# Performance work log

Hardware: AMD Instinct MI355X
Metric: run time of the kernel (lower is better)

The kernel has to match this reference:

```python
import jax, jax.numpy as jnp
import numpy as np

B, L, C, H = 8, 1024, 1024, 16  # batch, seq_len, n_embed, n_head


def setup_inputs() -> dict:
    key = jax.random.key(0)
    k0, k1, k2 = jax.random.split(key, 3)
    s = 0.02  # init scale
    return {
        "x": jax.random.normal(k0, (B, L, C), jnp.float32),
        "W_qkv": jax.random.normal(k1, (C, 3 * C), jnp.float32) * s,  # (in, out) layout
        "b_qkv": jnp.zeros((3 * C,), jnp.float32),
        "W_proj": jax.random.normal(k2, (C, C), jnp.float32) * s,
        "b_proj": jnp.zeros((C,), jnp.float32),
    }


def reference(x, W_qkv, b_qkv, W_proj, b_proj):
    Bb, Ll, Cc = x.shape
    d = Cc // H  # head dim
    qkv = x @ W_qkv + b_qkv                      # (B, L, 3C)
    q, k, v = jnp.split(qkv, 3, axis=2)
    q = q.reshape(Bb, Ll, H, d).transpose(0, 2, 1, 3)  # (B, H, L, d)
    k = k.reshape(Bb, Ll, H, d).transpose(0, 2, 1, 3)
    v = v.reshape(Bb, Ll, H, d).transpose(0, 2, 1, 3)
    scale = 1.0 / np.sqrt(d).astype(np.float32)
    attn = jnp.einsum("bhid,bhjd->bhij", q, k) * scale  # (B, H, Lq, Lk)
    causal = jnp.tril(jnp.ones((Ll, Ll), dtype=bool))    # (Lq, Lk)
    attn = jnp.where(causal[None, None, :, :], attn, -jnp.inf)
    # NOTE: source uses F.softmax(attn, dim=2) -> softmax over the QUERY axis.
    attn = jax.nn.softmax(attn, axis=2)
    y = jnp.einsum("bhij,bhjd->bhid", attn, v)           # (B, H, L, d)
    y = y.transpose(0, 2, 1, 3).reshape(Bb, Ll, Cc)      # (B, L, C)
    return y @ W_proj + b_proj
```

## Files before the change

### kernel.cpp

```cpp
#include <hip/hip_runtime.h>

typedef unsigned short u16;
typedef unsigned int   u32;
using bf16x8 = __attribute__((ext_vector_type(8))) short;
using f32x4  = __attribute__((ext_vector_type(4))) float;
using f32x16 = __attribute__((ext_vector_type(16))) float;
using u32x4  = __attribute__((ext_vector_type(4))) u32;

static constexpr int Bb = 8, Ll = 1024, Cc = 1024, Hh = 16, Dd = 64;
static constexpr int Mrows = Bb * Ll;
static constexpr int N3    = 3 * Cc;
static constexpr float QSCALE = 0.125f * 1.44269504088896f;

__device__ __forceinline__ u16 f2b(float f) {
    u32 u = __builtin_bit_cast(u32, f);
    u += 0x7FFFu + ((u >> 16) & 1u);
    return (u16)(u >> 16);
}
__device__ __forceinline__ float b2f(u16 u) {
    return __builtin_bit_cast(float, (u32)u << 16);
}
__device__ __forceinline__ u32 pack2bf(float a, float b) {
    return (u32)f2b(a) | ((u32)f2b(b) << 16);
}
__device__ __forceinline__ void gload16(const u16* g, u16* l) {
    __builtin_amdgcn_global_load_lds(
        (const __attribute__((address_space(1))) void*)g,
        (__attribute__((address_space(3))) void*)l, 16, 0, 0);
}

__global__ void k_f32_to_bf16(const float* __restrict__ in, u16* __restrict__ out, int n16) {
    int idx = blockIdx.x * blockDim.x + threadIdx.x;
    if (idx >= n16) return;
    #pragma unroll
    for (int h = 0; h < 2; ++h) {
        f32x4 v0 = *((const f32x4*)in + idx * 4 + h * 2);
        f32x4 v1 = *((const f32x4*)in + idx * 4 + h * 2 + 1);
        u32x4 o;
        o[0] = pack2bf(v0[0], v0[1]);
        o[1] = pack2bf(v0[2], v0[3]);
        o[2] = pack2bf(v1[0], v1[1]);
        o[3] = pack2bf(v1[2], v1[3]);
        *((u32x4*)out + idx * 2 + h) = o;
    }
}

__global__ void k_transpose_w(const float* __restrict__ Wqkv, u16* __restrict__ WqkvT,
                              const float* __restrict__ Wproj, u16* __restrict__ WprojT) {
    __shared__ float tile[32][33];
    int bx = blockIdx.x;
    const float* in; u16* out; int Cn;
    if (bx < 96) { in = Wqkv;  out = WqkvT;  Cn = N3; }
    else         { in = Wproj; out = WprojT; Cn = Cc; bx -= 96; }
    const int R = Cc;
    int tx = threadIdx.x, ty = threadIdx.y;
    int c = bx * 32 + tx;
    int rbase = blockIdx.y * 32;
    #pragma unroll
    for (int rr = 0; rr < 4; ++rr)
        tile[ty + rr * 8][tx] = in[(size_t)(rbase + ty + rr * 8) * Cn + c];
    __syncthreads();
    int ro = bx * 32 + ty;
    #pragma unroll
    for (int rr = 0; rr < 4; ++rr)
        out[(size_t)(ro + rr * 8) * R + rbase + tx] = f2b(tile[tx][ty + rr * 8]);
}

__global__ void k_transpose_scale_bf16(const u16* __restrict__ in, const float* __restrict__ zinv,
                                       u16* __restrict__ out, int R, int Cn) {
    __shared__ u16 tile[32][33];
    int bh = blockIdx.z;
    size_t base = (size_t)bh * R * Cn;
    int tx = threadIdx.x, ty = threadIdx.y;
    int c = blockIdx.x * 32 + tx;
    int rbase = blockIdx.y * 32;
    #pragma unroll
    for (int rr = 0; rr < 4; ++rr)
        tile[ty + rr * 8][tx] = in[base + (size_t)(rbase + ty + rr * 8) * Cn + c];
    __syncthreads();
    float zv = zinv[(size_t)bh * R + rbase + tx];
    int ro = blockIdx.x * 32 + ty;
    #pragma unroll
    for (int rr = 0; rr < 4; ++rr)
        out[base + (size_t)(ro + rr * 8) * R + rbase + tx] = f2b(b2f(tile[tx][ty + rr * 8]) * zv);
}

__global__ __launch_bounds__(256, 2)
void k_gemm_qkv32(const u16* __restrict__ A, const u16* __restrict__ Bt,
                  const float* __restrict__ bias,
                  u16* __restrict__ qo, u16* __restrict__ ko, u16* __restrict__ vo)
{
    const int K = Cc;
    const int NT = K / 64;
    __shared__ u16 As[2][128 * 64];
    __shared__ u16 Bs[2][128 * 64];
    const int tid = threadIdx.x;
    const int wid = tid >> 6, lane = tid & 63;
    const int l31 = lane & 31, lhi = lane >> 5, l7 = lane & 7;
    const int wr = wid >> 1, wc = wid & 1;
    const int nwg = gridDim.x * gridDim.y;
    const int flat = blockIdx.y * gridDim.x + blockIdx.x;
    const int swz = (flat & 7) * (nwg >> 3) + (flat >> 3);
    const int bx = swz % gridDim.x, by = swz / gridDim.x;
    const int row0 = by * 128, col0 = bx * 128;

    const int srow = tid >> 3;
    const int schunk = (tid & 7) ^ (srow & 7);
    const u16* gA = A  + (size_t)(row0 + srow) * K + schunk * 8;
    const u16* gB = Bt + (size_t)(col0 + srow) * K + schunk * 8;

#define STG(buf, t) do { \
    const u16* ga_ = gA + (size_t)(t) * 64; \
    const u16* gb_ = gB + (size_t)(t) * 64; \
    u16* la_ = &As[buf][wid * 512]; \
    u16* lb_ = &Bs[buf][wid * 512]; \
    gload16(ga_,                  la_); \
    gload16(ga_ + (size_t)32 * K, la_ + 2048); \
    gload16(ga_ + (size_t)64 * K, la_ + 4096); \
    gload16(ga_ + (size_t)96 * K, la_ + 6144); \
    gload16(gb_,                  lb_); \
    gload16(gb_ + (size_t)32 * K, lb_ + 2048); \
    gload16(gb_ + (size_t)64 * K, lb_ + 4096); \
    gload16(gb_ + (size_t)96 * K, lb_ + 6144); \
} while (0)

    const int coff0 = (((0 + lhi) ^ l7) << 3);
    const int coff1 = (((2 + lhi) ^ l7) << 3);
    const int coff2 = (((4 + lhi) ^ l7) << 3);
    const int coff3 = (((6 + lhi) ^ l7) << 3);
    const int coff[4] = { coff0, coff1, coff2, coff3 };

    f32x16 acc[2][2] = {};

    STG(0, 0);
    STG(1, 1);
    asm volatile("s_waitcnt vmcnt(8)" ::: "memory");
    __builtin_amdgcn_s_barrier();
    __builtin_amdgcn_sched_barrier(0);

    for (int t = 0; t < NT; ++t) {
        const u16* cA = &As[t & 1][0];
        const u16* cB = &Bs[t & 1][0];
        bf16x8 af[2][4], bf0[4];
        #pragma unroll
        for (int tm = 0; tm < 2; ++tm)
            #pragma unroll
            for (int kc = 0; kc < 4; ++kc)
                af[tm][kc] = *(const bf16x8*)&cA[(wr * 64 + tm * 32 + l31) * 64 + coff[kc]];
        #pragma unroll
        for (int kc = 0; kc < 4; ++kc)
            bf0[kc] = *(const bf16x8*)&cB[(wc * 64 + l31) * 64 + coff[kc]];
        __builtin_amdgcn_s_setprio(1);
        #pragma unroll
        for (int tm = 0; tm < 2; ++tm)
            #pragma unroll
            for (int kc = 0; kc < 4; ++kc)
                acc[tm][0] = __builtin_amdgcn_mfma_f32_32x32x16_bf16(
                    af[tm][kc], bf0[kc], acc[tm][0], 0, 0, 0);
        __builtin_amdgcn_s_setprio(0);
        __builtin_amdgcn_s_barrier();
        bf16x8 bf1[4];
        #pragma unroll
        for (int kc = 0; kc < 4; ++kc)
            bf1[kc] = *(const bf16x8*)&cB[(wc * 64 + 32 + l31) * 64 + coff[kc]];
        __builtin_amdgcn_s_setprio(1);
        #pragma unroll
        for (int tm = 0; tm < 2; ++tm)
            #pragma unroll
            for (int kc = 0; kc < 4; ++kc)
                acc[tm][1] = __builtin_amdgcn_mfma_f32_32x32x16_bf16(
                    af[tm][kc], bf1[kc], acc[tm][1], 0, 0, 0);
        __builtin_amdgcn_s_setprio(0);
        __builtin_amdgcn_s_barrier();
        __builtin_amdgcn_sched_barrier(0);
        if (t + 2 < NT) STG(t & 1, t + 2);
        if (t + 1 < NT) {
            if (t + 2 < NT) { asm volatile("s_waitcnt vmcnt(8)" ::: "memory"); }
            else            { asm volatile("s_waitcnt vmcnt(0)" ::: "memory"); }
            __builtin_amdgcn_s_barrier();
            __builtin_amdgcn_sched_barrier(0);
        }
    }
#undef STG

    #pragma unroll
    for (int tm = 0; tm < 2; ++tm) {
        #pragma unroll
        for (int tn = 0; tn < 2; ++tn) {
            int cg = col0 + wc * 64 + tn * 32 + l31;
            float bv = bias[cg];
            int which = cg >> 10;
            float sc = (which == 0) ? QSCALE : 1.0f;
            int cc2 = cg & 1023;
            int h = cc2 >> 6, dd = cc2 & 63;
            int rbase = row0 + wr * 64 + tm * 32 + 4 * lhi;
            #pragma unroll
            for (int g = 0; g < 4; ++g) {
                #pragma unroll
                for (int r = 0; r < 4; ++r) {
                    int rg = rbase + 8 * g + r;
                    int bidx = rg >> 10, ll2 = rg & 1023;
                    size_t o = ((size_t)(bidx * Hh + h) * Ll + ll2) * Dd + dd;
                    u16 val = f2b((acc[tm][tn][g * 4 + r] + bv) * sc);
                    if (which == 0) qo[o] = val;
                    else if (which == 1) ko[o] = val;
                    else vo[o] = val;
                }
            }
        }
    }
}

__global__ __launch_bounds__(256)
void k_gemm_proj(const u16* __restrict__ A, const u16* __restrict__ Bt,
                 const float* __restrict__ bias, float* __restrict__ outf)
{
    const int N = Cc, K = Cc;
    __shared__ u16 As[2][128 * 32];
    __shared__ u16 Bs[2][128 * 32];
    const int tid = threadIdx.x;
    const int wid = tid >> 6, lane = tid & 63;
    const int lr = lane & 15, lg = lane >> 4;
    const int wr = wid >> 1, wc = wid & 1;
    const int nwg = gridDim.x * gridDim.y;
    const int flat = blockIdx.y * gridDim.x + blockIdx.x;
    const int swz = (flat & 7) * (nwg >> 3) + (flat >> 3);
    const int bx = swz % gridDim.x, by = swz / gridDim.x;
    const int row0 = by * 128, col0 = bx * 128;

    const int srow = wid * 32 + (lane >> 2);
    const int schk = (lane & 3) ^ (srow & 3);
    const u16* aP = A  + (size_t)(row0 + srow) * K + schk * 8;
    const u16* bP = Bt + (size_t)(col0 + srow) * K + schk * 8;
    const size_t r16 = (size_t)16 * K;
    u16* aL0 = &As[0][wid * 32 * 32]; u16* aL0b = aL0 + 16 * 32;
    u16* bL0 = &Bs[0][wid * 32 * 32]; u16* bL0b = bL0 + 16 * 32;
    u16* aL1 = &As[1][wid * 32 * 32]; u16* aL1b = aL1 + 16 * 32;
    u16* bL1 = &Bs[1][wid * 32 * 32]; u16* bL1b = bL1 + 16 * 32;

    f32x4 acc[4][4] = {};

#define STAGE0(kk) { gload16(aP + (kk), aL0); gload16(aP + r16 + (kk), aL0b); \
                     gload16(bP + (kk), bL0); gload16(bP + r16 + (kk), bL0b); }
#define STAGE1(kk) { gload16(aP + (kk), aL1); gload16(aP + r16 + (kk), aL1b); \
                     gload16(bP + (kk), bL1); gload16(bP + r16 + (kk), bL1b); }
#define COMPUTE(bufi) { \
        bf16x8 af[4], bfv[4]; \
        _Pragma("unroll") \
        for (int m = 0; m < 4; ++m) { int rw = wr * 64 + m * 16 + lr; \
            af[m] = *(const bf16x8*)&As[bufi][rw * 32 + ((lg ^ (rw & 3)) * 8)]; } \
        _Pragma("unroll") \
        for (int n = 0; n < 4; ++n) { int rw = wc * 64 + n * 16 + lr; \
            bfv[n] = *(const bf16x8*)&Bs[bufi][rw * 32 + ((lg ^ (rw & 3)) * 8)]; } \
        _Pragma("unroll") \
        for (int m = 0; m < 4; ++m) \
            _Pragma("unroll") \
            for (int n = 0; n < 4; ++n) \
                acc[m][n] = __builtin_amdgcn_mfma_f32_16x16x32_bf16(af[m], bfv[n], acc[m][n], 0, 0, 0); }

    STAGE0(0);
    __syncthreads();
    for (int k0 = 0; k0 < K; k0 += 64) {
        if (k0 + 32 < K) STAGE1(k0 + 32);
        COMPUTE(0);
        __syncthreads();
        if (k0 + 64 < K) STAGE0(k0 + 64);
        COMPUTE(1);
        __syncthreads();
    }
#undef STAGE0
#undef STAGE1
#undef COMPUTE

    #pragma unroll
    for (int m = 0; m < 4; ++m) {
        int rb2 = row0 + wr * 64 + m * 16 + lg * 4;
        #pragma unroll
        for (int n = 0; n < 4; ++n) {
            int cg = col0 + wc * 64 + n * 16 + lr;
            float bv = bias[cg];
            #pragma unroll
            for (int r = 0; r < 4; ++r)
                outf[(size_t)(rb2 + r) * N + cg] = acc[m][n][r] + bv;
        }
    }
}

__global__ __launch_bounds__(256, 4)
void k_attn_colsum(const u16* __restrict__ Q, const u16* __restrict__ Kb,
                   float* __restrict__ zinv)
{
    __shared__ u16 Qs[2][64 * 64];
    const int tid = threadIdx.x;
    const int wid = tid >> 6, lane = tid & 63;
    const int lr = lane & 15, lg = lane >> 4;
    const int l7 = lr & 7;
    const int fid = blockIdx.x;
    const int xcd = fid & 7, n = fid >> 3;
    const int xtA = n & 7;
    const int xtB = 15 - xtA;
    const int bh = (xcd << 4) | (n >> 3);
    const u16* Qp = Q  + (size_t)bh * Ll * Dd;
    const u16* Kp = Kb + (size_t)bh * Ll * Dd;
    const int jwA = xtA * 64 + wid * 16;
    const int jwB = xtB * 64 + wid * 16;
    bf16x8 kbA0 = *(const bf16x8*)&Kp[(jwA + lr) * Dd + lg * 8];
    bf16x8 kbA1 = *(const bf16x8*)&Kp[(jwA + lr) * Dd + 32 + lg * 8];
    bf16x8 kbB0 = *(const bf16x8*)&Kp[(jwB + lr) * Dd + lg * 8];
    bf16x8 kbB1 = *(const bf16x8*)&Kp[(jwB + lr) * Dd + 32 + lg * 8];
    const bool dmask[4] = { lg * 4 + 0 >= lr, lg * 4 + 1 >= lr,
                            lg * 4 + 2 >= lr, lg * 4 + 3 >= lr };
    const int ch0 = ((lg ^ l7) << 3);
    const int ch1 = (((4 + lg) ^ l7) << 3);
    const int srow = tid >> 3;
    const int schunk = (tid & 7) ^ (srow & 7);
    float zA = 0.f, zB = 0.f;

    const int nA = 16 - xtA;
    const int NS = 17;
#define IOF(s) (((s) < nA) ? (xtA * 64 + 64 * (s)) : (xtB * 64 + 64 * ((s) - nA)))

#define STGQ(buf, I0) do { \
    const u16* g_ = Qp + (size_t)((I0) + srow) * 64 + schunk * 8; \
    u16* l_ = &Qs[buf][wid * 512]; \
    gload16(g_,                   l_); \
    gload16(g_ + (size_t)32 * 64, l_ + 2048); \
} while (0)

#define CS_STEP(buf, I0, JW, KB0, KB1, ZACC) do { \
    const u16* Qs_ = &Qs[buf][0]; \
    _Pragma("unroll") \
    for (int ss = 0; ss < 4; ++ss) { \
        int ib = (I0) + ss * 16; \
        if (ib >= (JW)) { \
            bf16x8 qa0 = *(const bf16x8*)&Qs_[(ss * 16 + lr) * 64 + ch0]; \
            bf16x8 qa1 = *(const bf16x8*)&Qs_[(ss * 16 + lr) * 64 + ch1]; \
            f32x4 s_ = {0.f, 0.f, 0.f, 0.f}; \
            s_ = __builtin_amdgcn_mfma_f32_16x16x32_bf16(qa0, KB0, s_, 0, 0, 0); \
            s_ = __builtin_amdgcn_mfma_f32_16x16x32_bf16(qa1, KB1, s_, 0, 0, 0); \
            if (ib >= (JW) + 16) { \
                _Pragma("unroll") \
                for (int r = 0; r < 4; ++r) ZACC += exp2f(s_[r]); \
            } else { \
                _Pragma("unroll") \
                for (int r = 0; r < 4; ++r) ZACC += dmask[r] ? exp2f(s_[r]) : 0.f; \
            } \
        } \
    } \
} while (0)

    STGQ(0, IOF(0));
    STGQ(1, IOF(1));
    asm volatile("s_waitcnt vmcnt(2)" ::: "memory");
    __builtin_amdgcn_s_barrier();
    __builtin_amdgcn_sched_barrier(0);

    for (int s = 0; s < NS; ++s) {
        if (s < nA) { CS_STEP((s & 1), xtA * 64 + 64 * s, jwA, kbA0, kbA1, zA); }
        else        { CS_STEP((s & 1), xtB * 64 + 64 * (s - nA), jwB, kbB0, kbB1, zB); }
        __builtin_amdgcn_s_barrier();
        __builtin_amdgcn_sched_barrier(0);
        if (s + 2 < NS) STGQ((s & 1), IOF(s + 2));
        if (s + 1 < NS) {
            if (s + 2 < NS) { asm volatile("s_waitcnt vmcnt(2)" ::: "memory"); }
            else            { asm volatile("s_waitcnt vmcnt(0)" ::: "memory"); }
            __builtin_amdgcn_s_barrier();
            __builtin_amdgcn_sched_barrier(0);
        }
    }
#undef STGQ
#undef CS_STEP
#undef IOF

    zA += __shfl_xor(zA, 16); zA += __shfl_xor(zA, 32);
    zB += __shfl_xor(zB, 16); zB += __shfl_xor(zB, 32);
    if (lg == 0) {
        zinv[(size_t)bh * Ll + jwA + lr] = 1.f / zA;
        zinv[(size_t)bh * Ll + jwB + lr] = 1.f / zB;
    }
}

__global__ __launch_bounds__(256, 4)
void k_attn_pv(const u16* __restrict__ Q, const u16* __restrict__ Kb,
               const u16* __restrict__ Vt, u16* __restrict__ Y)
{
    __shared__ u16 Ks[2][64 * 64];
    __shared__ u16 Vs[2][64 * 64];
    const int tid = threadIdx.x;
    const int wid = tid >> 6, lane = tid & 63;
    const int lr = lane & 15, lg = lane >> 4;
    const int l7 = lr & 7;
    const int fid = blockIdx.x;
    const int xcd = fid & 7, n = fid >> 3;
    const int xtA = n & 7;
    const int xtB = 15 - xtA;
    const int bh = (xcd << 4) | (n >> 3);
    const int bidx = bh >> 4, h = bh & 15;
    const u16* Qp = Q  + (size_t)bh * Ll * Dd;
    const u16* Kp = Kb + (size_t)bh * Ll * Dd;
    const u16* Vp = Vt + (size_t)bh * Ll * Dd;
    const int src0 = lr + 32 * (lg & 1);
    const int src1 = src0 + 16;
    const bool selHi = (lg & 2) != 0;
    const int ch0 = ((lg ^ l7) << 3);
    const int ch1 = (((4 + lg) ^ l7) << 3);
    const int srow = tid >> 3;
    const int schunk = (tid & 7) ^ (srow & 7);

    const int iwA = xtA * 64 + wid * 16;
    const int iwB = xtB * 64 + wid * 16;
    bf16x8 qaA0 = *(const bf16x8*)&Qp[(iwA + lr) * Dd + lg * 8];
    bf16x8 qaA1 = *(const bf16x8*)&Qp[(iwA + lr) * Dd + 32 + lg * 8];
    bf16x8 qaB0 = *(const bf16x8*)&Qp[(iwB + lr) * Dd + lg * 8];
    bf16x8 qaB1 = *(const bf16x8*)&Qp[(iwB + lr) * Dd + 32 + lg * 8];
    f32x4 yaccA[4] = {};
    f32x4 yaccB[4] = {};

    const int NS = 17;
#define JOF(s) (((s) <= xtA) ? 64 * (s) : 64 * ((s) - xtA - 1))

#define STGKV(buf, J) do { \
    const u16* gk_ = Kp + (size_t)((J) + srow) * 64 + schunk * 8; \
    const u16* gv_ = Vp + (size_t)srow * Ll + (J) + schunk * 8; \
    u16* lk_ = &Ks[buf][wid * 512]; \
    u16* lv_ = &Vs[buf][wid * 512]; \
    gload16(gk_,                   lk_); \
    gload16(gk_ + (size_t)32 * 64, lk_ + 2048); \
    gload16(gv_,                   lv_); \
    gload16(gv_ + (size_t)32 * Ll, lv_ + 2048); \
} while (0)

#define PV_STEP(buf, J0, IW, QA0, QA1, YACC) do { \
    const u16* Ks_ = &Ks[buf][0]; \
    const u16* Vs_ = &Vs[buf][0]; \
    uint2 w0, w1, w2, w3; \
    _Pragma("unroll") \
    for (int cs = 0; cs < 4; ++cs) { \
        bf16x8 kb0 = *(const bf16x8*)&Ks_[(cs * 16 + lr) * 64 + ch0]; \
        bf16x8 kb1 = *(const bf16x8*)&Ks_[(cs * 16 + lr) * 64 + ch1]; \
        f32x4 s_ = {0.f, 0.f, 0.f, 0.f}; \
        s_ = __builtin_amdgcn_mfma_f32_16x16x32_bf16(kb0, QA0, s_, 0, 0, 0); \
        s_ = __builtin_amdgcn_mfma_f32_16x16x32_bf16(kb1, QA1, s_, 0, 0, 0); \
        int jb = (J0) + cs * 16; \
        float p[4]; \
        if (jb + 15 <= (IW)) { \
            _Pragma("unroll") \
            for (int r = 0; r < 4; ++r) p[r] = exp2f(s_[r]); \
        } else { \
            int ig = (IW) + lr; \
            _Pragma("unroll") \
            for (int r = 0; r < 4; ++r) \
                p[r] = (jb + 4 * lg + r <= ig) ? exp2f(s_[r]) : 0.f; \
        } \
        uint2 w_; \
        w_.x = pack2bf(p[0], p[1]); \
        w_.y = pack2bf(p[2], p[3]); \
        if (cs == 0) w0 = w_; else if (cs == 1) w1 = w_; \
        else if (cs == 2) w2 = w_; else w3 = w_; \
    } \
    u32 a00 = (u32)__shfl((int)w0.x, src0), a01 = (u32)__shfl((int)w0.y, src0); \
    u32 a02 = (u32)__shfl((int)w0.x, src1), a03 = (u32)__shfl((int)w0.y, src1); \
    u32 a10 = (u32)__shfl((int)w1.x, src0), a11 = (u32)__shfl((int)w1.y, src0); \
    u32 a12 = (u32)__shfl((int)w1.x, src1), a13 = (u32)__shfl((int)w1.y, src1); \
    u32 a20 = (u32)__shfl((int)w2.x, src0), a21 = (u32)__shfl((int)w2.y, src0); \
    u32 a22 = (u32)__shfl((int)w2.x, src1), a23 = (u32)__shfl((int)w2.y, src1); \
    u32 a30 = (u32)__shfl((int)w3.x, src0), a31 = (u32)__shfl((int)w3.y, src0); \
    u32 a32 = (u32)__shfl((int)w3.x, src1), a33 = (u32)__shfl((int)w3.y, src1); \
    u32x4 pa0u, pa1u; \
    pa0u[0] = selHi ? a10 : a00;  pa0u[1] = selHi ? a11 : a01; \
    pa0u[2] = selHi ? a12 : a02;  pa0u[3] = selHi ? a13 : a03; \
    pa1u[0] = selHi ? a30 : a20;  pa1u[1] = selHi ? a31 : a21; \
    pa1u[2] = selHi ? a32 : a22;  pa1u[3] = selHi ? a33 : a23; \
    bf16x8 pa0 = __builtin_bit_cast(bf16x8, pa0u); \
    bf16x8 pa1 = __builtin_bit_cast(bf16x8, pa1u); \
    _Pragma("unroll") \
    for (int ns = 0; ns < 4; ++ns) { \
        bf16x8 vb0 = *(const bf16x8*)&Vs_[(ns * 16 + lr) * 64 + ch0]; \
        bf16x8 vb1 = *(const bf16x8*)&Vs_[(ns * 16 + lr) * 64 + ch1]; \
        YACC[ns] = __builtin_amdgcn_mfma_f32_16x16x32_bf16(pa0, vb0, YACC[ns], 0, 0, 0); \
        YACC[ns] = __builtin_amdgcn_mfma_f32_16x16x32_bf16(pa1, vb1, YACC[ns], 0, 0, 0); \
    } \
} while (0)

    STGKV(0, 0);
    STGKV(1, JOF(1));
    asm volatile("s_waitcnt vmcnt(4)" ::: "memory");
    __builtin_amdgcn_s_barrier();
    __builtin_amdgcn_sched_barrier(0);

    for (int s = 0; s < NS; ++s) {
        if (s <= xtA) { PV_STEP((s & 1), 64 * s, iwA, qaA0, qaA1, yaccA); }
        else          { PV_STEP((s & 1), 64 * (s - xtA - 1), iwB, qaB0, qaB1, yaccB); }
        __builtin_amdgcn_s_barrier();
        __builtin_amdgcn_sched_barrier(0);
        if (s + 2 < NS) STGKV((s & 1), JOF(s + 2));
        if (s + 1 < NS) {
            if (s + 2 < NS) { asm volatile("s_waitcnt vmcnt(4)" ::: "memory"); }
            else            { asm volatile("s_waitcnt vmcnt(0)" ::: "memory"); }
            __builtin_amdgcn_s_barrier();
            __builtin_amdgcn_sched_barrier(0);
        }
    }
#undef STGKV
#undef PV_STEP
#undef JOF

    #pragma unroll
    for (int ns = 0; ns < 4; ++ns)
        #pragma unroll
        for (int r = 0; r < 4; ++r) {
            int l2 = iwA + lg * 4 + r;
            Y[((size_t)bidx * Ll + l2) * Cc + h * Dd + ns * 16 + lr] = f2b(yaccA[ns][r]);
        }
    #pragma unroll
    for (int ns = 0; ns < 4; ++ns)
        #pragma unroll
        for (int r = 0; r < 4; ++r) {
            int l2 = iwB + lg * 4 + r;
            Y[((size_t)bidx * Ll + l2) * Cc + h * Dd + ns * 16 + lr] = f2b(yaccB[ns][r]);
        }
}

extern "C" void kernel_launch(void* const* d_in, const int* in_sizes, int n_in,
                              void* d_out, int out_size, void* d_ws, size_t ws_size,
                              hipStream_t stream)
{
    const float* x     = (const float*)d_in[0];
    const float* Wqkv  = (const float*)d_in[1];
    const float* bqkv  = (const float*)d_in[2];
    const float* Wproj = (const float*)d_in[3];
    const float* bproj = (const float*)d_in[4];
    float* out = (float*)d_out;

    char* ws = (char*)d_ws;
    u16* xb     = (u16*)(ws + 0);
    u16* WqkvT  = (u16*)(ws + 16777216);
    u16* WprojT = (u16*)(ws + 23068672);
    u16* q      = (u16*)(ws + 25165824);
    u16* k      = (u16*)(ws + 41943040);
    u16* v      = (u16*)(ws + 58720256);
    u16* vt     = (u16*)(ws + 75497472);
    float* zinv = (float*)(ws + 92274688);

    k_f32_to_bf16<<<dim3(2048), dim3(256), 0, stream>>>(x, xb, Mrows * Cc / 16);
    k_transpose_w<<<dim3(128, 32), dim3(32, 8), 0, stream>>>(Wqkv, WqkvT, Wproj, WprojT);
    k_gemm_qkv32<<<dim3(N3 / 128, Mrows / 128), dim3(256), 0, stream>>>(
        xb, WqkvT, bqkv, q, k, v);
    k_attn_colsum<<<dim3(1024), dim3(256), 0, stream>>>(q, k, zinv);
    k_transpose_scale_bf16<<<dim3(2, 32, Bb * Hh), dim3(32, 8), 0, stream>>>(v, zinv, vt, Ll, Dd);
    k_attn_pv<<<dim3(1024), dim3(256), 0, stream>>>(q, k, vt, v);
    k_gemm_proj<<<dim3(Cc / 128, Mrows / 128), dim3(256), 0, stream>>>(
        v, WprojT, bproj, out);
}
```

Before: 188.8 us.

## Rewrite projection GEMM with 32x32x16 MFMA and K=64 double-buffered tiles

Replaces the output projection GEMM's 16x16x32 MFMA inner loop with 32x32x16 MFMAs and switches from K=32 to K=64 LDS tiles with an 8-chunk XOR swizzle. Loads are issued two tiles ahead, with explicit vmcnt waits, raw s_barrier and setprio around the MFMA bursts, mirroring the existing QKV GEMM. The aim is fewer LDS reads per flop and better overlap of global loads with compute. The cost is double the LDS per block and tighter occupancy (launch bounds 256,2).

```diff
diff --git a/kernel.cpp b/kernel.cpp
--- a/kernel.cpp
+++ b/kernel.cpp
@@ -211,16 +211,18 @@
     }
 }
 
-__global__ __launch_bounds__(256)
-void k_gemm_proj(const u16* __restrict__ A, const u16* __restrict__ Bt,
-                 const float* __restrict__ bias, float* __restrict__ outf)
+__global__ __launch_bounds__(256, 2)
+void k_gemm_proj32(const u16* __restrict__ A, const u16* __restrict__ Bt,
+                   const float* __restrict__ bias, float* __restrict__ outf)
 {
-    const int N = Cc, K = Cc;
-    __shared__ u16 As[2][128 * 32];
-    __shared__ u16 Bs[2][128 * 32];
+    const int K = Cc;
+    const int N = Cc;
+    const int NT = K / 64;
+    __shared__ u16 As[2][128 * 64];
+    __shared__ u16 Bs[2][128 * 64];
     const int tid = threadIdx.x;
     const int wid = tid >> 6, lane = tid & 63;
-    const int lr = lane & 15, lg = lane >> 4;
+    const int l31 = lane & 31, lhi = lane >> 5, l7 = lane & 7;
     const int wr = wid >> 1, wc = wid & 1;
     const int nwg = gridDim.x * gridDim.y;
     const int flat = blockIdx.y * gridDim.x + blockIdx.x;
@@ -228,60 +230,100 @@
     const int bx = swz % gridDim.x, by = swz / gridDim.x;
     const int row0 = by * 128, col0 = bx * 128;
 
-    const int srow = wid * 32 + (lane >> 2);
-    const int schk = (lane & 3) ^ (srow & 3);
-    const u16* aP = A  + (size_t)(row0 + srow) * K + schk * 8;
-    const u16* bP = Bt + (size_t)(col0 + srow) * K + schk * 8;
-    const size_t r16 = (size_t)16 * K;
-    u16* aL0 = &As[0][wid * 32 * 32]; u16* aL0b = aL0 + 16 * 32;
-    u16* bL0 = &Bs[0][wid * 32 * 32]; u16* bL0b = bL0 + 16 * 32;
-    u16* aL1 = &As[1][wid * 32 * 32]; u16* aL1b = aL1 + 16 * 32;
-    u16* bL1 = &Bs[1][wid * 32 * 32]; u16* bL1b = bL1 + 16 * 32;
-
-    f32x4 acc[4][4] = {};
-
-#define STAGE0(kk) { gload16(aP + (kk), aL0); gload16(aP + r16 + (kk), aL0b); \
-                     gload16(bP + (kk), bL0); gload16(bP + r16 + (kk), bL0b); }
-#define STAGE1(kk) { gload16(aP + (kk), aL1); gload16(aP + r16 + (kk), aL1b); \
-                     gload16(bP + (kk), bL1); gload16(bP + r16 + (kk), bL1b); }
-#define COMPUTE(bufi) { \
-        bf16x8 af[4], bfv[4]; \
-        _Pragma("unroll") \
-        for (int m = 0; m < 4; ++m) { int rw = wr * 64 + m * 16 + lr; \
-            af[m] = *(const bf16x8*)&As[bufi][rw * 32 + ((lg ^ (rw & 3)) * 8)]; } \
-        _Pragma("unroll") \
-        for (int n = 0; n < 4; ++n) { int rw = wc * 64 + n * 16 + lr; \
-            bfv[n] = *(const bf16x8*)&Bs[bufi][rw * 32 + ((lg ^ (rw & 3)) * 8)]; } \
-        _Pragma("unroll") \
-        for (int m = 0; m < 4; ++m) \
-            _Pragma("unroll") \
-            for (int n = 0; n < 4; ++n) \
-                acc[m][n] = __builtin_amdgcn_mfma_f32_16x16x32_bf16(af[m], bfv[n], acc[m][n], 0, 0, 0); }
-
-    STAGE0(0);
-    __syncthreads();
-    for (int k0 = 0; k0 < K; k0 += 64) {
-        if (k0 + 32 < K) STAGE1(k0 + 32);
-        COMPUTE(0);
-        __syncthreads();
-        if (k0 + 64 < K) STAGE0(k0 + 64);
-        COMPUTE(1);
-        __syncthreads();
-    }
-#undef STAGE0
-#undef STAGE1
-#undef COMPUTE
-
-    #pragma unroll
-    for (int m = 0; m < 4; ++m) {
-        int rb2 = row0 + wr * 64 + m * 16 + lg * 4;
-        #pragma unroll
-        for (int n = 0; n < 4; ++n) {
-            int cg = col0 + wc * 64 + n * 16 + lr;
+    const int srow = tid >> 3;
+    const int schunk = (tid & 7) ^ (srow & 7);
+    const u16* gA = A  + (size_t)(row0 + srow) * K + schunk * 8;
+    const u16* gB = Bt + (size_t)(col0 + srow) * K + schunk * 8;
+
+#define STG(buf, t) do { \
+    const u16* ga_ = gA + (size_t)(t) * 64; \
+    const u16* gb_ = gB + (size_t)(t) * 64; \
+    u16* la_ = &As[buf][wid * 512]; \
+    u16* lb_ = &Bs[buf][wid * 512]; \
+    gload16(ga_,                  la_); \
+    gload16(ga_ + (size_t)32 * K, la_ + 2048); \
+    gload16(ga_ + (size_t)64 * K, la_ + 4096); \
+    gload16(ga_ + (size_t)96 * K, la_ + 6144); \
+    gload16(gb_,                  lb_); \
+    gload16(gb_ + (size_t)32 * K, lb_ + 2048); \
+    gload16(gb_ + (size_t)64 * K, lb_ + 4096); \
+    gload16(gb_ + (size_t)96 * K, lb_ + 6144); \
+} while (0)
+
+    const int coff0 = (((0 + lhi) ^ l7) << 3);
+    const int coff1 = (((2 + lhi) ^ l7) << 3);
+    const int coff2 = (((4 + lhi) ^ l7) << 3);
+    const int coff3 = (((6 + lhi) ^ l7) << 3);
+    const int coff[4] = { coff0, coff1, coff2, coff3 };
+
+    f32x16 acc[2][2] = {};
+
+    STG(0, 0);
+    STG(1, 1);
+    asm volatile("s_waitcnt vmcnt(8)" ::: "memory");
+    __builtin_amdgcn_s_barrier();
+    __builtin_amdgcn_sched_barrier(0);
+
+    for (int t = 0; t < NT; ++t) {
+        const u16* cA = &As[t & 1][0];
+        const u16* cB = &Bs[t & 1][0];
+        bf16x8 af[2][4], bf0[4];
+        #pragma unroll
+        for (int tm = 0; tm < 2; ++tm)
+            #pragma unroll
+            for (int kc = 0; kc < 4; ++kc)
+                af[tm][kc] = *(const bf16x8*)&cA[(wr * 64 + tm * 32 + l31) * 64 + coff[kc]];
+        #pragma unroll
+        for (int kc = 0; kc < 4; ++kc)
+            bf0[kc] = *(const bf16x8*)&cB[(wc * 64 + l31) * 64 + coff[kc]];
+        __builtin_amdgcn_s_setprio(1);
+        #pragma unroll
+        for (int tm = 0; tm < 2; ++tm)
+            #pragma unroll
+            for (int kc = 0; kc < 4; ++kc)
+                acc[tm][0] = __builtin_amdgcn_mfma_f32_32x32x16_bf16(
+                    af[tm][kc], bf0[kc], acc[tm][0], 0, 0, 0);
+        __builtin_amdgcn_s_setprio(0);
+        __builtin_amdgcn_s_barrier();
+        bf16x8 bf1[4];
+        #pragma unroll
+        for (int kc = 0; kc < 4; ++kc)
+            bf1[kc] = *(const bf16x8*)&cB[(wc * 64 + 32 + l31) * 64 + coff[kc]];
+        __builtin_amdgcn_s_setprio(1);
+        #pragma unroll
+        for (int tm = 0; tm < 2; ++tm)
+            #pragma unroll
+            for (int kc = 0; kc < 4; ++kc)
+                acc[tm][1] = __builtin_amdgcn_mfma_f32_32x32x16_bf16(
+                    af[tm][kc], bf1[kc], acc[tm][1], 0, 0, 0);
+        __builtin_amdgcn_s_setprio(0);
+        __builtin_amdgcn_s_barrier();
+        __builtin_amdgcn_sched_barrier(0);
+        if (t + 2 < NT) STG(t & 1, t + 2);
+        if (t + 1 < NT) {
+            if (t + 2 < NT) { asm volatile("s_waitcnt vmcnt(8)" ::: "memory"); }
+            else            { asm volatile("s_waitcnt vmcnt(0)" ::: "memory"); }
+            __builtin_amdgcn_s_barrier();
+            __builtin_amdgcn_sched_barrier(0);
+        }
+    }
+#undef STG
+
+    #pragma unroll
+    for (int tm = 0; tm < 2; ++tm) {
+        #pragma unroll
+        for (int tn = 0; tn < 2; ++tn) {
+            int cg = col0 + wc * 64 + tn * 32 + l31;
             float bv = bias[cg];
-            #pragma unroll
-            for (int r = 0; r < 4; ++r)
-                outf[(size_t)(rb2 + r) * N + cg] = acc[m][n][r] + bv;
+            int rbase = row0 + wr * 64 + tm * 32 + 4 * lhi;
+            #pragma unroll
+            for (int g = 0; g < 4; ++g) {
+                #pragma unroll
+                for (int r = 0; r < 4; ++r) {
+                    int rg = rbase + 8 * g + r;
+                    outf[(size_t)rg * N + cg] = acc[tm][tn][g * 4 + r] + bv;
+                }
+            }
         }
     }
 }
@@ -549,6 +591,6 @@
     k_attn_colsum<<<dim3(1024), dim3(256), 0, stream>>>(q, k, zinv);
     k_transpose_scale_bf16<<<dim3(2, 32, Bb * Hh), dim3(32, 8), 0, stream>>>(v, zinv, vt, Ll, Dd);
     k_attn_pv<<<dim3(1024), dim3(256), 0, stream>>>(q, k, vt, v);
-    k_gemm_proj<<<dim3(Cc / 128, Mrows / 128), dim3(256), 0, stream>>>(
+    k_gemm_proj32<<<dim3(Cc / 128, Mrows / 128), dim3(256), 0, stream>>>(
         v, WprojT, bproj, out);
 }
```

After: 183.9 us. 2.6% less time.
